# Performance work log

Measured on AMD Instinct MI355X. Metric: run time of the kernel, lower is better.

## Reference

```python
import jax, jax.numpy as jnp
import numpy as np
import math

B, S, D, H, DFF = 2, 2048, 1024, 16, 4096
DK = D // H
EPS = 1e-5


def setup_inputs() -> dict:
    key = jax.random.key(0)
    ks = jax.random.split(key, 8)
    s = 0.02
    return {
        "x": jax.random.normal(ks[0], (B, S, D), jnp.float32),
        "wq": jax.random.normal(ks[1], (D, D), jnp.float32) * s,
        "bq": jnp.zeros((D,), jnp.float32),
        "wk": jax.random.normal(ks[2], (D, D), jnp.float32) * s,
        "bk": jnp.zeros((D,), jnp.float32),
        "wv": jax.random.normal(ks[3], (D, D), jnp.float32) * s,
        "bv": jnp.zeros((D,), jnp.float32),
        "wo": jax.random.normal(ks[4], (D, D), jnp.float32) * s,
        "bo": jnp.zeros((D,), jnp.float32),
        "g1": jnp.ones((D,), jnp.float32),
        "beta1": jnp.zeros((D,), jnp.float32),
        "w1": jax.random.normal(ks[5], (D, DFF), jnp.float32) * s,
        "b1": jnp.zeros((DFF,), jnp.float32),
        "w2": jax.random.normal(ks[6], (DFF, D), jnp.float32) * s,
        "b2": jnp.zeros((D,), jnp.float32),
        "g2": jnp.ones((D,), jnp.float32),
        "beta2": jnp.zeros((D,), jnp.float32),
    }


def _layernorm(x, g, b):
    m = jnp.mean(x, axis=-1, keepdims=True)
    v = jnp.mean(jnp.square(x - m), axis=-1, keepdims=True)
    return (x - m) * jax.lax.rsqrt(v + EPS) * g + b


def reference(x, wq, bq, wk, bk, wv, bv, wo, bo, g1, beta1, w1, b1, w2, b2, g2, beta2):
    b, s, _ = x.shape
    # QKV projections -> [b, h, s, dk]
    q = (x @ wq + bq).reshape(b, s, H, DK).transpose(0, 2, 1, 3)
    k = (x @ wk + bk).reshape(b, s, H, DK).transpose(0, 2, 1, 3)
    v = (x @ wv + bv).reshape(b, s, H, DK).transpose(0, 2, 1, 3)
    scores = jnp.einsum('bhqd,bhkd->bhqk', q, k) / math.sqrt(DK)  # [b,h,s,s]
    # Faithful to source: softmax over dim=1 (heads axis), not the key axis.
    attn = jax.nn.softmax(scores, axis=1)
    ctx = jnp.einsum('bhqk,bhkd->bhqd', attn, v)
    ctx = ctx.transpose(0, 2, 1, 3).reshape(b, s, D)
    attn_out = ctx @ wo + bo
    # dropout is identity in eval mode
    x1 = _layernorm(x + attn_out, g1, beta1)
    ff = jax.nn.relu(x1 @ w1 + b1) @ w2 + b2
    return _layernorm(x1 + ff, g2, beta2)
```

## Files before the change

### kernel.cpp

```cpp
#include <hip/hip_runtime.h>
#include <stdint.h>

#define B_   2
#define S_   2048
#define D_   1024
#define H_   16
#define DK_  64
#define DFF_ 4096
#define M_   (B_ * S_)
#define QKV_LD 3072

typedef unsigned short u16;
typedef unsigned int   u32;
typedef __attribute__((ext_vector_type(8))) short short8;
typedef __attribute__((ext_vector_type(4))) float f32x4;

__device__ __forceinline__ float b2f(u16 u) {
  union { u32 i; float f; } z; z.i = ((u32)u) << 16; return z.f;
}
__device__ __forceinline__ u16 f2b(float f) {
  union { float f; u32 i; } z; z.f = f;
  u32 x = z.i;
  u32 r = (x + 0x7fffu + ((x >> 16) & 1u)) >> 16;
  return (u16)r;
}
__device__ __forceinline__ void load4(const float* p, float* f) {
  float4 v = *(const float4*)p;
  f[0] = v.x; f[1] = v.y; f[2] = v.z; f[3] = v.w;
}
__device__ __forceinline__ void load4(const u16* p, float* f) {
  uint2 v = *(const uint2*)p;
  f[0] = b2f(v.x & 0xffffu); f[1] = b2f(v.x >> 16);
  f[2] = b2f(v.y & 0xffffu); f[3] = b2f(v.y >> 16);
}
__device__ __forceinline__ void tstore(float* p, float v) { *p = v; }
__device__ __forceinline__ void tstore(u16* p, float v)   { *p = f2b(v); }

__device__ __forceinline__ void gld_lds16(const void* g, void* l) {
  __builtin_amdgcn_global_load_lds(
      (const __attribute__((address_space(1))) void*)g,
      (__attribute__((address_space(3))) void*)l, 16, 0, 0);
}

template<int BM, bool RELU, bool RES, bool BIAS, bool QKV, typename TO>
__global__ __launch_bounds__(256)
void gemm_bf16(const u16* __restrict__ A, const u16* __restrict__ Wt,
               const float* __restrict__ bias0, const float* __restrict__ bias1,
               const float* __restrict__ bias2, const float* __restrict__ res,
               TO* __restrict__ C, int M, int N, int K)
{
  constexpr int WM = BM / 2;
  constexpr int MI = WM / 16;
  __shared__ u16 As[BM][32];
  __shared__ u16 Bs[128][32];

  const int tid  = threadIdx.x;
  const int wave = tid >> 6;
  const int lane = tid & 63;
  const int lo16 = lane & 15;
  const int quad = lane >> 4;
  const int row0 = blockIdx.y * BM;
  const int col0 = blockIdx.x * 128;
  const int mb   = (wave & 1) * WM;
  const int nb   = (wave >> 1) * 64;

  const float* bias = bias0;
  float osc = 1.0f;
  if (QKV) {
    const int seg = col0 >> 10;
    bias = (seg == 0) ? bias0 : (seg == 1 ? bias1 : bias2);
    if (seg == 0) osc = 0.125f;
  }
  const int bc0 = QKV ? (col0 & 1023) : col0;

  f32x4 acc[MI][4];
#pragma unroll
  for (int i = 0; i < MI; ++i)
#pragma unroll
    for (int j = 0; j < 4; ++j) acc[i][j] = (f32x4){0.f, 0.f, 0.f, 0.f};

  const int s_row = tid >> 2;
  const int s_ch  = (tid & 3) * 8;
  const u16* gA = A  + (size_t)(row0 + s_row) * K + s_ch;
  const u16* gB = Wt + (size_t)(col0 + s_row) * K + s_ch;

  for (int k0 = 0; k0 < K; k0 += 32) {
    gld_lds16(gA, &As[s_row][s_ch]);
    if constexpr (BM == 128)
      gld_lds16(gA + (size_t)64 * K, &As[s_row + (BM == 128 ? 64 : 0)][s_ch]);
    gld_lds16(gB, &Bs[s_row][s_ch]);
    gld_lds16(gB + (size_t)64 * K, &Bs[s_row + 64][s_ch]);
    gA += 32; gB += 32;
    __syncthreads();

    short8 af[MI], bf[4];
#pragma unroll
    for (int mi = 0; mi < MI; ++mi)
      af[mi] = *(const short8*)&As[mb + mi * 16 + lo16][quad * 8];
#pragma unroll
    for (int ni = 0; ni < 4; ++ni)
      bf[ni] = *(const short8*)&Bs[nb + ni * 16 + lo16][quad * 8];
#pragma unroll
    for (int mi = 0; mi < MI; ++mi)
#pragma unroll
      for (int ni = 0; ni < 4; ++ni)
        acc[mi][ni] = __builtin_amdgcn_mfma_f32_16x16x32_bf16(af[mi], bf[ni], acc[mi][ni], 0, 0, 0);
    __syncthreads();
  }

  float bv[4];
#pragma unroll
  for (int ni = 0; ni < 4; ++ni)
    bv[ni] = BIAS ? bias[bc0 + nb + ni * 16 + lo16] : 0.f;
#pragma unroll
  for (int mi = 0; mi < MI; ++mi) {
#pragma unroll
    for (int ni = 0; ni < 4; ++ni) {
      const int col = col0 + nb + ni * 16 + lo16;
#pragma unroll
      for (int r = 0; r < 4; ++r) {
        const int row = row0 + mb + mi * 16 + quad * 4 + r;
        float vv = (acc[mi][ni][r] + bv[ni]) * osc;
        if (RELU) vv = fmaxf(vv, 0.f);
        if (RES)  vv += res[(size_t)row * N + col];
        tstore(C + (size_t)row * N + col, vv);
      }
    }
  }
}

__global__ __launch_bounds__(256)
void cvt_f2b(const float* __restrict__ in, u16* __restrict__ out)
{
  const size_t i = ((size_t)blockIdx.x * 256 + threadIdx.x) * 8;
  float4 a = *(const float4*)(in + i);
  float4 b = *(const float4*)(in + i + 4);
  uint4 o;
  o.x = (u32)f2b(a.x) | ((u32)f2b(a.y) << 16);
  o.y = (u32)f2b(a.z) | ((u32)f2b(a.w) << 16);
  o.z = (u32)f2b(b.x) | ((u32)f2b(b.y) << 16);
  o.w = (u32)f2b(b.z) | ((u32)f2b(b.w) << 16);
  *(uint4*)(out + i) = o;
}

__global__ __launch_bounds__(256)
void merge_b16(const u16* __restrict__ p0, const u16* __restrict__ p1,
               u16* __restrict__ out)
{
  const size_t i = ((size_t)blockIdx.x * 256 + threadIdx.x) * 8;
  uint4 a = *(const uint4*)(p0 + i);
  uint4 b = *(const uint4*)(p1 + i);
  uint4 o;
  const u32* ap = (const u32*)&a;
  const u32* bp = (const u32*)&b;
  u32* op = (u32*)&o;
#pragma unroll
  for (int j = 0; j < 4; ++j) {
    float lo = b2f((u16)(ap[j] & 0xffffu)) + b2f((u16)(bp[j] & 0xffffu));
    float hi = b2f((u16)(ap[j] >> 16))     + b2f((u16)(bp[j] >> 16));
    op[j] = (u32)f2b(lo) | ((u32)f2b(hi) << 16);
  }
  *(uint4*)(out + i) = o;
}

__global__ __launch_bounds__(256)
void transpose_f2b(const float* __restrict__ in, u16* __restrict__ out,
                   int ld_in, int ld_out)
{
  __shared__ u16 tile[64][68];
  const int t  = threadIdx.x;
  const int r0 = blockIdx.x * 64;
  const int c0 = blockIdx.y * 64;
  const int rr = t >> 4;
  const int cc = (t & 15) * 4;
#pragma unroll
  for (int rep = 0; rep < 4; ++rep) {
    float4 v = *(const float4*)(in + (size_t)(r0 + rr + rep * 16) * ld_in + c0 + cc);
    tile[rr + rep * 16][cc + 0] = f2b(v.x);
    tile[rr + rep * 16][cc + 1] = f2b(v.y);
    tile[rr + rep * 16][cc + 2] = f2b(v.z);
    tile[rr + rep * 16][cc + 3] = f2b(v.w);
  }
  __syncthreads();
#pragma unroll
  for (int rep = 0; rep < 4; ++rep) {
    const int dr = rr + rep * 16;
    uint2 o;
    o.x = (u32)tile[cc + 0][dr] | ((u32)tile[cc + 1][dr] << 16);
    o.y = (u32)tile[cc + 2][dr] | ((u32)tile[cc + 3][dr] << 16);
    *(uint2*)(out + (size_t)(c0 + dr) * ld_out + r0 + cc) = o;
  }
}

__global__ __launch_bounds__(256)
void transpose_bf16(const u16* __restrict__ in, u16* __restrict__ out,
                    int ld_in, int ld_out)
{
  __shared__ u16 tile[64][68];
  const int t  = threadIdx.x;
  const int r0 = blockIdx.x * 64;
  const int c0 = blockIdx.y * 64;
  const int rr = t >> 4;
  const int cc = (t & 15) * 4;
#pragma unroll
  for (int rep = 0; rep < 4; ++rep) {
    uint2 vv = *(const uint2*)(in + (size_t)(r0 + rr + rep * 16) * ld_in + c0 + cc);
    *(uint2*)&tile[rr + rep * 16][cc] = vv;
  }
  __syncthreads();
#pragma unroll
  for (int rep = 0; rep < 4; ++rep) {
    const int dr = rr + rep * 16;
    uint2 o;
    o.x = (u32)tile[cc + 0][dr] | ((u32)tile[cc + 1][dr] << 16);
    o.y = (u32)tile[cc + 2][dr] | ((u32)tile[cc + 3][dr] << 16);
    *(uint2*)(out + (size_t)(c0 + dr) * ld_out + r0 + cc) = o;
  }
}

__device__ __forceinline__ short8 scale8(short8 a, f32x4 r0, f32x4 r1) {
  const u32* ap = (const u32*)&a;
  short8 o;
  u32* op = (u32*)&o;
#pragma unroll
  for (int i = 0; i < 4; ++i) {
    union { u32 u; float f; } lo, hi;
    lo.u = ap[i] << 16;
    hi.u = ap[i] & 0xffff0000u;
    float rl = (i < 2) ? r0[2 * i]     : r1[2 * i - 4];
    float rh = (i < 2) ? r0[2 * i + 1] : r1[2 * i - 3];
    lo.f *= rl;
    hi.f *= rh;
    op[i] = ((lo.u + 0x8000u) >> 16) | ((hi.u + 0x8000u) & 0xffff0000u);
  }
  return o;
}

__global__ __launch_bounds__(512, 2)
void attention_mfma(const u16* __restrict__ q, const u16* __restrict__ k,
                    const u16* __restrict__ vt, u16* __restrict__ partial)
{
  __shared__ __align__(16) u16 Ws[16][32][64];
  __shared__ __align__(16) float Rs[32][64];

  const int tid  = threadIdx.x;
  const int wave = tid >> 6;
  const int lane = tid & 63;
  const int lo16 = lane & 15;
  const int quad = lane >> 4;

  const int p     = blockIdx.x;
  const int g     = (p & 7) >> 1;
  const int batch = g >> 1;
  const int half  = g & 1;
  const int qt    = ((p >> 3) << 1) | (p & 1);
  const int qrow0 = batch * S_ + qt * 32;
  const int tbase = half * 1024;

  const int qg = wave >> 2;
  const int tg = wave & 3;
  const int h0 = wave * 2;

  const u16* qrow = q + (size_t)(qrow0 + qg * 16 + lo16) * QKV_LD + quad * 8;
  short8 qf[32];
#pragma unroll
  for (int h = 0; h < 16; ++h) {
    qf[2 * h]     = *(const short8*)(qrow + h * 64);
    qf[2 * h + 1] = *(const short8*)(qrow + h * 64 + 32);
  }

  f32x4 acc[2][2][4];
#pragma unroll
  for (int a = 0; a < 2; ++a)
#pragma unroll
    for (int b = 0; b < 2; ++b)
#pragma unroll
      for (int c = 0; c < 4; ++c) acc[a][b][c] = (f32x4){0.f, 0.f, 0.f, 0.f};

  const u16* kbase = k + (size_t)(batch * S_ + tbase + tg * 16 + lo16) * QKV_LD + quad * 8;
  const u16* vbase0 = vt + (size_t)batch * S_ + tbase + quad * 8;

  int pos_r[4], qabs_r[4];
#pragma unroll
  for (int r = 0; r < 4; ++r) {
    qabs_r[r] = qg * 16 + quad * 4 + r;
    pos_r[r]  = (tg * 16 + lo16) ^ ((qabs_r[r] & 7) << 3);
  }

  for (int s = 0; s < 16; ++s) {
    {
      const u16* krow = kbase + (size_t)(s * 64) * QKV_LD;
      float ssum[4] = {0.f, 0.f, 0.f, 0.f};
#pragma unroll
      for (int h = 0; h < 16; ++h) {
        short8 b0 = *(const short8*)(krow + h * 64);
        short8 b1 = *(const short8*)(krow + h * 64 + 32);
        f32x4 sg = (f32x4){0.f, 0.f, 0.f, 0.f};
        sg = __builtin_amdgcn_mfma_f32_16x16x32_bf16(qf[2 * h],     b0, sg, 0, 0, 0);
        sg = __builtin_amdgcn_mfma_f32_16x16x32_bf16(qf[2 * h + 1], b1, sg, 0, 0, 0);
#pragma unroll
        for (int r = 0; r < 4; ++r) {
          union { float f; u32 u; } e;
          e.f = __expf(sg[r]);
          ssum[r] += e.f;
          Ws[h][qabs_r[r]][pos_r[r]] = (u16)((e.u + 0x8000u) >> 16);
        }
      }
#pragma unroll
      for (int r = 0; r < 4; ++r)
        Rs[qabs_r[r]][pos_r[r]] = 1.0f / ssum[r];
    }
    __syncthreads();

#pragma unroll
    for (int kc = 0; kc < 2; ++kc) {
      const int kbaseT = kc * 32 + quad * 8;
      const int ksw    = kbaseT ^ ((lo16 & 7) << 3);
      f32x4 rv0a = *(const f32x4*)&Rs[lo16][ksw];
      f32x4 rv0b = *(const f32x4*)&Rs[lo16][ksw + 4];
      f32x4 rv1a = *(const f32x4*)&Rs[16 + lo16][ksw];
      f32x4 rv1b = *(const f32x4*)&Rs[16 + lo16][ksw + 4];
#pragma unroll
      for (int hh = 0; hh < 2; ++hh) {
        short8 sw0 = scale8(*(const short8*)&Ws[h0 + hh][lo16][ksw],      rv0a, rv0b);
        short8 sw1 = scale8(*(const short8*)&Ws[h0 + hh][16 + lo16][ksw], rv1a, rv1b);
#pragma unroll
        for (int dt = 0; dt < 4; ++dt) {
          short8 bv = *(const short8*)(vbase0 +
              (size_t)((h0 + hh) * 64 + dt * 16 + lo16) * M_ + s * 64 + kc * 32);
          acc[hh][0][dt] = __builtin_amdgcn_mfma_f32_16x16x32_bf16(sw0, bv, acc[hh][0][dt], 0, 0, 0);
          acc[hh][1][dt] = __builtin_amdgcn_mfma_f32_16x16x32_bf16(sw1, bv, acc[hh][1][dt], 0, 0, 0);
        }
      }
    }
    __syncthreads();
  }

  u16* pb = partial + (size_t)half * M_ * D_;
#pragma unroll
  for (int hh = 0; hh < 2; ++hh)
#pragma unroll
    for (int qgg = 0; qgg < 2; ++qgg)
#pragma unroll
      for (int dt = 0; dt < 4; ++dt)
#pragma unroll
        for (int r = 0; r < 4; ++r) {
          const int row = qrow0 + qgg * 16 + quad * 4 + r;
          const int col = (h0 + hh) * 64 + dt * 16 + lo16;
          pb[(size_t)row * D_ + col] = f2b(acc[hh][qgg][dt][r]);
        }
}

__device__ __forceinline__ float block_sum(float vv, float* sm) {
#pragma unroll
  for (int o = 32; o > 0; o >>= 1) vv += __shfl_down(vv, o);
  __syncthreads();
  if ((threadIdx.x & 63) == 0) sm[threadIdx.x >> 6] = vv;
  __syncthreads();
  return sm[0] + sm[1] + sm[2] + sm[3];
}

template<bool HAS_Y, bool AUX>
__global__ __launch_bounds__(256)
void add_ln(const float* __restrict__ x, const u16* __restrict__ y,
            const float* __restrict__ g, const float* __restrict__ bta,
            float* __restrict__ out, u16* __restrict__ aux)
{
  __shared__ float sm[4];
  const int row = blockIdx.x;
  const int t   = threadIdx.x;
  const size_t base = (size_t)row * D_ + t * 4;

  float s[4];
  load4(x + base, s);
  if (HAS_Y) {
    float yv[4];
    load4(y + base, yv);
    s[0] += yv[0]; s[1] += yv[1]; s[2] += yv[2]; s[3] += yv[3];
  }

  float loc = s[0] + s[1] + s[2] + s[3];
  float tot = block_sum(loc, sm);
  float mean = tot * (1.f / 1024.f);
  float d0 = s[0] - mean, d1 = s[1] - mean, d2 = s[2] - mean, d3 = s[3] - mean;
  float sq = d0 * d0 + d1 * d1 + d2 * d2 + d3 * d3;
  float tv = block_sum(sq, sm);
  float rstd = rsqrtf(tv * (1.f / 1024.f) + 1e-5f);

  float4 gv = *(const float4*)(g + t * 4);
  float4 bv = *(const float4*)(bta + t * 4);
  float o0 = d0 * rstd * gv.x + bv.x;
  float o1 = d1 * rstd * gv.y + bv.y;
  float o2 = d2 * rstd * gv.z + bv.z;
  float o3 = d3 * rstd * gv.w + bv.w;
  *(float4*)(out + base) = make_float4(o0, o1, o2, o3);
  if (AUX) {
    uint2 ov;
    ov.x = (u32)f2b(o0) | ((u32)f2b(o1) << 16);
    ov.y = (u32)f2b(o2) | ((u32)f2b(o3) << 16);
    *(uint2*)(aux + base) = ov;
  }
}

extern "C" void kernel_launch(void* const* d_in, const int* in_sizes, int n_in,
                              void* d_out, int out_size, void* d_ws, size_t ws_size,
                              hipStream_t stream) {
  const float* x     = (const float*)d_in[0];
  const float* wq    = (const float*)d_in[1];
  const float* bq    = (const float*)d_in[2];
  const float* wk    = (const float*)d_in[3];
  const float* bk    = (const float*)d_in[4];
  const float* wv    = (const float*)d_in[5];
  const float* bv    = (const float*)d_in[6];
  const float* wo    = (const float*)d_in[7];
  const float* bo    = (const float*)d_in[8];
  const float* g1    = (const float*)d_in[9];
  const float* beta1 = (const float*)d_in[10];
  const float* w1    = (const float*)d_in[11];
  const float* b1    = (const float*)d_in[12];
  const float* w2    = (const float*)d_in[13];
  const float* b2    = (const float*)d_in[14];
  const float* g2    = (const float*)d_in[15];
  const float* beta2 = (const float*)d_in[16];
  float* outF = (float*)d_out;

  char* wsb = (char*)d_ws;
  const size_t MiB = (size_t)1 << 20;
  u16* qkv   = (u16*)(wsb + 0);
  u16* wqkvt = (u16*)(wsb + 24 * MiB);
  u16* vt    = (u16*)(wsb + 24 * MiB);
  u16* ctx_b = (u16*)(wsb + 0);
  u16* ao    = (u16*)(wsb + 8 * MiB);
  u16* wot   = (u16*)(wsb + 16 * MiB);
  u16* x1b   = (u16*)(wsb + 0);
  u16* w1t   = (u16*)(wsb + 8 * MiB);
  u16* w2t   = (u16*)(wsb + 12 * MiB);
  u16* h1    = (u16*)(wsb + 16 * MiB);
  u16* xb    = (u16*)d_out;
  u16* part  = (u16*)d_out;
  float* x1  = outF;
  float* z   = outF;

  dim3 blk(256);
  cvt_f2b<<<dim3((M_ * D_) / (256 * 8)), blk, 0, stream>>>(x, xb);
  transpose_f2b<<<dim3(16, 16), blk, 0, stream>>>(wq, wqkvt,                 D_, D_);
  transpose_f2b<<<dim3(16, 16), blk, 0, stream>>>(wk, wqkvt + 1024 * 1024,   D_, D_);
  transpose_f2b<<<dim3(16, 16), blk, 0, stream>>>(wv, wqkvt + 2048 * 1024,   D_, D_);
  gemm_bf16<128, false, false, true, true, u16><<<dim3(QKV_LD / 128, M_ / 128), blk, 0, stream>>>(
      xb, wqkvt, bq, bk, bv, nullptr, qkv, M_, QKV_LD, D_);
  transpose_bf16<<<dim3(M_ / 64, 1024 / 64), blk, 0, stream>>>(qkv + 2048, vt, QKV_LD, M_);
  attention_mfma<<<dim3(256), dim3(512), 0, stream>>>(qkv, qkv + 1024, vt, part);
  merge_b16<<<dim3((M_ * D_) / (256 * 8)), blk, 0, stream>>>(part, part + (size_t)M_ * D_, ctx_b);
  transpose_f2b<<<dim3(16, 16), blk, 0, stream>>>(wo, wot, D_, D_);
  gemm_bf16<64, false, false, true, false, u16><<<dim3(D_ / 128, M_ / 64), blk, 0, stream>>>(
      ctx_b, wot, bo, nullptr, nullptr, nullptr, ao, M_, D_, D_);
  add_ln<true, true><<<dim3(M_), blk, 0, stream>>>(x, ao, g1, beta1, x1, x1b);
  transpose_f2b<<<dim3(16, 32), blk, 0, stream>>>(w1, w1t, DFF_, D_);
  transpose_f2b<<<dim3(32, 16), blk, 0, stream>>>(w2, w2t, D_, 2048);
  gemm_bf16<128, true, false, true, false, u16><<<dim3(2048 / 128, M_ / 128), blk, 0, stream>>>(
      x1b, w1t, b1, nullptr, nullptr, nullptr, h1, M_, 2048, D_);
  gemm_bf16<64, false, true, false, false, float><<<dim3(D_ / 128, M_ / 64), blk, 0, stream>>>(
      h1, w2t, nullptr, nullptr, nullptr, x1, z, M_, D_, 2048);
  transpose_f2b<<<dim3(16, 32), blk, 0, stream>>>(w1 + 2048, w1t, DFF_, D_);
  transpose_f2b<<<dim3(32, 16), blk, 0, stream>>>(w2 + (size_t)2048 * 1024, w2t, D_, 2048);
  gemm_bf16<128, true, false, true, false, u16><<<dim3(2048 / 128, M_ / 128), blk, 0, stream>>>(
      x1b, w1t, b1 + 2048, nullptr, nullptr, nullptr, h1, M_, 2048, D_);
  gemm_bf16<64, false, true, true, false, float><<<dim3(D_ / 128, M_ / 64), blk, 0, stream>>>(
      h1, w2t, b2, nullptr, nullptr, z, z, M_, D_, 2048);
  add_ln<false, false><<<dim3(M_), blk, 0, stream>>>(z, nullptr, g2, beta2, outF, nullptr);
}
```

Before: 594.4 us.

## Shrink attention blocks to 16 query rows and double-buffer softmax tiles

The attention kernel now launches 512 blocks of 256 threads instead of 256 blocks of 512. Each block handles 16 query rows, and each wave covers 4 heads instead of 2 heads by 2 row groups. The exp-weight and reciprocal shared-memory tiles are double-buffered, so the next key tile's QK MFMA and exp work is issued before the current tile's PV accumulation, with one barrier per iteration instead of two. This aims to overlap the two phases and use more CUs, at the cost of reading each K/V tile twice as often overall.

```diff
diff --git a/kernel.cpp b/kernel.cpp
--- a/kernel.cpp
+++ b/kernel.cpp
@@ -236,12 +236,12 @@
   return o;
 }
 
-__global__ __launch_bounds__(512, 2)
+__global__ __launch_bounds__(256, 2)
 void attention_mfma(const u16* __restrict__ q, const u16* __restrict__ k,
                     const u16* __restrict__ vt, u16* __restrict__ partial)
 {
-  __shared__ __align__(16) u16 Ws[16][32][64];
-  __shared__ __align__(16) float Rs[32][64];
+  __shared__ __align__(16) u16 Ws[2][16][16][64];
+  __shared__ __align__(16) float Rs[2][16][64];
 
   const int tid  = threadIdx.x;
   const int wave = tid >> 6;
@@ -254,14 +254,13 @@
   const int batch = g >> 1;
   const int half  = g & 1;
   const int qt    = ((p >> 3) << 1) | (p & 1);
-  const int qrow0 = batch * S_ + qt * 32;
+  const int qrow0 = batch * S_ + qt * 16;
   const int tbase = half * 1024;
 
-  const int qg = wave >> 2;
-  const int tg = wave & 3;
-  const int h0 = wave * 2;
-
-  const u16* qrow = q + (size_t)(qrow0 + qg * 16 + lo16) * QKV_LD + quad * 8;
+  const int tg = wave;
+  const int h0 = wave * 4;
+
+  const u16* qrow = q + (size_t)(qrow0 + lo16) * QKV_LD + quad * 8;
   short8 qf[32];
 #pragma unroll
   for (int h = 0; h < 16; ++h) {
@@ -269,67 +268,65 @@
     qf[2 * h + 1] = *(const short8*)(qrow + h * 64 + 32);
   }
 
-  f32x4 acc[2][2][4];
-#pragma unroll
-  for (int a = 0; a < 2; ++a)
-#pragma unroll
-    for (int b = 0; b < 2; ++b)
-#pragma unroll
-      for (int c = 0; c < 4; ++c) acc[a][b][c] = (f32x4){0.f, 0.f, 0.f, 0.f};
+  f32x4 acc[4][4];
+#pragma unroll
+  for (int a = 0; a < 4; ++a)
+#pragma unroll
+    for (int c = 0; c < 4; ++c) acc[a][c] = (f32x4){0.f, 0.f, 0.f, 0.f};
 
   const u16* kbase = k + (size_t)(batch * S_ + tbase + tg * 16 + lo16) * QKV_LD + quad * 8;
-  const u16* vbase0 = vt + (size_t)batch * S_ + tbase + quad * 8;
+  const u16* vb    = vt + (size_t)batch * S_ + tbase + quad * 8;
 
   int pos_r[4], qabs_r[4];
 #pragma unroll
   for (int r = 0; r < 4; ++r) {
-    qabs_r[r] = qg * 16 + quad * 4 + r;
+    qabs_r[r] = quad * 4 + r;
     pos_r[r]  = (tg * 16 + lo16) ^ ((qabs_r[r] & 7) << 3);
   }
 
+  auto phaseA = [&](int s, int buf) {
+    const u16* krow = kbase + (size_t)(s * 64) * QKV_LD;
+    float ssum[4] = {0.f, 0.f, 0.f, 0.f};
+#pragma unroll
+    for (int h = 0; h < 16; ++h) {
+      short8 b0 = *(const short8*)(krow + h * 64);
+      short8 b1 = *(const short8*)(krow + h * 64 + 32);
+      f32x4 sg = (f32x4){0.f, 0.f, 0.f, 0.f};
+      sg = __builtin_amdgcn_mfma_f32_16x16x32_bf16(qf[2 * h],     b0, sg, 0, 0, 0);
+      sg = __builtin_amdgcn_mfma_f32_16x16x32_bf16(qf[2 * h + 1], b1, sg, 0, 0, 0);
+#pragma unroll
+      for (int r = 0; r < 4; ++r) {
+        union { float f; u32 u; } e;
+        e.f = __expf(sg[r]);
+        ssum[r] += e.f;
+        Ws[buf][h][qabs_r[r]][pos_r[r]] = (u16)((e.u + 0x8000u) >> 16);
+      }
+    }
+#pragma unroll
+    for (int r = 0; r < 4; ++r)
+      Rs[buf][qabs_r[r]][pos_r[r]] = 1.0f / ssum[r];
+  };
+
+  phaseA(0, 0);
+  __syncthreads();
+
   for (int s = 0; s < 16; ++s) {
-    {
-      const u16* krow = kbase + (size_t)(s * 64) * QKV_LD;
-      float ssum[4] = {0.f, 0.f, 0.f, 0.f};
-#pragma unroll
-      for (int h = 0; h < 16; ++h) {
-        short8 b0 = *(const short8*)(krow + h * 64);
-        short8 b1 = *(const short8*)(krow + h * 64 + 32);
-        f32x4 sg = (f32x4){0.f, 0.f, 0.f, 0.f};
-        sg = __builtin_amdgcn_mfma_f32_16x16x32_bf16(qf[2 * h],     b0, sg, 0, 0, 0);
-        sg = __builtin_amdgcn_mfma_f32_16x16x32_bf16(qf[2 * h + 1], b1, sg, 0, 0, 0);
-#pragma unroll
-        for (int r = 0; r < 4; ++r) {
-          union { float f; u32 u; } e;
-          e.f = __expf(sg[r]);
-          ssum[r] += e.f;
-          Ws[h][qabs_r[r]][pos_r[r]] = (u16)((e.u + 0x8000u) >> 16);
-        }
-      }
-#pragma unroll
-      for (int r = 0; r < 4; ++r)
-        Rs[qabs_r[r]][pos_r[r]] = 1.0f / ssum[r];
-    }
-    __syncthreads();
+    const int buf = s & 1;
+    if (s < 15) phaseA(s + 1, buf ^ 1);
 
 #pragma unroll
     for (int kc = 0; kc < 2; ++kc) {
-      const int kbaseT = kc * 32 + quad * 8;
-      const int ksw    = kbaseT ^ ((lo16 & 7) << 3);
-      f32x4 rv0a = *(const f32x4*)&Rs[lo16][ksw];
-      f32x4 rv0b = *(const f32x4*)&Rs[lo16][ksw + 4];
-      f32x4 rv1a = *(const f32x4*)&Rs[16 + lo16][ksw];
-      f32x4 rv1b = *(const f32x4*)&Rs[16 + lo16][ksw + 4];
-#pragma unroll
-      for (int hh = 0; hh < 2; ++hh) {
-        short8 sw0 = scale8(*(const short8*)&Ws[h0 + hh][lo16][ksw],      rv0a, rv0b);
-        short8 sw1 = scale8(*(const short8*)&Ws[h0 + hh][16 + lo16][ksw], rv1a, rv1b);
+      const int ksw = (kc * 32 + quad * 8) ^ ((lo16 & 7) << 3);
+      f32x4 rva = *(const f32x4*)&Rs[buf][lo16][ksw];
+      f32x4 rvb = *(const f32x4*)&Rs[buf][lo16][ksw + 4];
+#pragma unroll
+      for (int hh = 0; hh < 4; ++hh) {
+        short8 aw = scale8(*(const short8*)&Ws[buf][h0 + hh][lo16][ksw], rva, rvb);
 #pragma unroll
         for (int dt = 0; dt < 4; ++dt) {
-          short8 bv = *(const short8*)(vbase0 +
+          short8 bv = *(const short8*)(vb +
               (size_t)((h0 + hh) * 64 + dt * 16 + lo16) * M_ + s * 64 + kc * 32);
-          acc[hh][0][dt] = __builtin_amdgcn_mfma_f32_16x16x32_bf16(sw0, bv, acc[hh][0][dt], 0, 0, 0);
-          acc[hh][1][dt] = __builtin_amdgcn_mfma_f32_16x16x32_bf16(sw1, bv, acc[hh][1][dt], 0, 0, 0);
+          acc[hh][dt] = __builtin_amdgcn_mfma_f32_16x16x32_bf16(aw, bv, acc[hh][dt], 0, 0, 0);
         }
       }
     }
@@ -338,17 +335,15 @@
 
   u16* pb = partial + (size_t)half * M_ * D_;
 #pragma unroll
-  for (int hh = 0; hh < 2; ++hh)
-#pragma unroll
-    for (int qgg = 0; qgg < 2; ++qgg)
-#pragma unroll
-      for (int dt = 0; dt < 4; ++dt)
-#pragma unroll
-        for (int r = 0; r < 4; ++r) {
-          const int row = qrow0 + qgg * 16 + quad * 4 + r;
-          const int col = (h0 + hh) * 64 + dt * 16 + lo16;
-          pb[(size_t)row * D_ + col] = f2b(acc[hh][qgg][dt][r]);
-        }
+  for (int hh = 0; hh < 4; ++hh)
+#pragma unroll
+    for (int dt = 0; dt < 4; ++dt)
+#pragma unroll
+      for (int r = 0; r < 4; ++r) {
+        const int row = qrow0 + quad * 4 + r;
+        const int col = (h0 + hh) * 64 + dt * 16 + lo16;
+        pb[(size_t)row * D_ + col] = f2b(acc[hh][dt][r]);
+      }
 }
 
 __device__ __forceinline__ float block_sum(float vv, float* sm) {
@@ -449,7 +444,7 @@
   gemm_bf16<128, false, false, true, true, u16><<<dim3(QKV_LD / 128, M_ / 128), blk, 0, stream>>>(
       xb, wqkvt, bq, bk, bv, nullptr, qkv, M_, QKV_LD, D_);
   transpose_bf16<<<dim3(M_ / 64, 1024 / 64), blk, 0, stream>>>(qkv + 2048, vt, QKV_LD, M_);
-  attention_mfma<<<dim3(256), dim3(512), 0, stream>>>(qkv, qkv + 1024, vt, part);
+  attention_mfma<<<dim3(512), dim3(256), 0, stream>>>(qkv, qkv + 1024, vt, part);
   merge_b16<<<dim3((M_ * D_) / (256 * 8)), blk, 0, stream>>>(part, part + (size_t)M_ * D_, ctx_b);
   transpose_f2b<<<dim3(16, 16), blk, 0, stream>>>(wo, wot, D_, D_);
   gemm_bf16<64, false, false, true, false, u16><<<dim3(D_ / 128, M_ / 64), blk, 0, stream>>>(
```

Result: slower. 657.5 us (+10.6%).

## Double-buffer attention score tiles and prefetch next K block during PV

Applied to the files above, without the earlier changes.

Splits the attention loop into a software pipeline. The exp-score tile and reciprocal sums for step s+1 are computed into a second LDS buffer while step s's buffer feeds the PV MFMAs, and next-step K fragments are loaded into registers before the PV work. This removes one barrier per iteration and aims to overlap K global loads and score MFMAs with PV compute. In exchange it doubles LDS use to about 147KB, which likely prevents two blocks per CU. It also adds 32 short8 registers of K fragments, which may cause spills.

```diff
diff --git a/kernel.cpp b/kernel.cpp
--- a/kernel.cpp
+++ b/kernel.cpp
@@ -240,8 +240,8 @@
 void attention_mfma(const u16* __restrict__ q, const u16* __restrict__ k,
                     const u16* __restrict__ vt, u16* __restrict__ partial)
 {
-  __shared__ __align__(16) u16 Ws[16][32][64];
-  __shared__ __align__(16) float Rs[32][64];
+  __shared__ __align__(16) u16 Ws[2][16][32][64];
+  __shared__ __align__(16) float Rs[2][32][64];
 
   const int tid  = threadIdx.x;
   const int wave = tid >> 6;
@@ -277,7 +277,7 @@
 #pragma unroll
       for (int c = 0; c < 4; ++c) acc[a][b][c] = (f32x4){0.f, 0.f, 0.f, 0.f};
 
-  const u16* kbase = k + (size_t)(batch * S_ + tbase + tg * 16 + lo16) * QKV_LD + quad * 8;
+  const u16* kbase  = k + (size_t)(batch * S_ + tbase + tg * 16 + lo16) * QKV_LD + quad * 8;
   const u16* vbase0 = vt + (size_t)batch * S_ + tbase + quad * 8;
 
   int pos_r[4], qabs_r[4];
@@ -287,43 +287,54 @@
     pos_r[r]  = (tg * 16 + lo16) ^ ((qabs_r[r] & 7) << 3);
   }
 
+  {
+    const u16* krow = kbase;
+    float ssum[4] = {0.f, 0.f, 0.f, 0.f};
+#pragma unroll
+    for (int h = 0; h < 16; ++h) {
+      short8 b0 = *(const short8*)(krow + h * 64);
+      short8 b1 = *(const short8*)(krow + h * 64 + 32);
+      f32x4 sg = (f32x4){0.f, 0.f, 0.f, 0.f};
+      sg = __builtin_amdgcn_mfma_f32_16x16x32_bf16(qf[2 * h],     b0, sg, 0, 0, 0);
+      sg = __builtin_amdgcn_mfma_f32_16x16x32_bf16(qf[2 * h + 1], b1, sg, 0, 0, 0);
+#pragma unroll
+      for (int r = 0; r < 4; ++r) {
+        union { float f; u32 u; } e;
+        e.f = __expf(sg[r]);
+        ssum[r] += e.f;
+        Ws[0][h][qabs_r[r]][pos_r[r]] = (u16)((e.u + 0x8000u) >> 16);
+      }
+    }
+#pragma unroll
+    for (int r = 0; r < 4; ++r)
+      Rs[0][qabs_r[r]][pos_r[r]] = 1.0f / ssum[r];
+  }
+  __syncthreads();
+
   for (int s = 0; s < 16; ++s) {
-    {
-      const u16* krow = kbase + (size_t)(s * 64) * QKV_LD;
-      float ssum[4] = {0.f, 0.f, 0.f, 0.f};
+    const int buf = s & 1;
+
+    short8 kf[32];
+    if (s < 15) {
+      const u16* krow = kbase + (size_t)((s + 1) * 64) * QKV_LD;
 #pragma unroll
       for (int h = 0; h < 16; ++h) {
-        short8 b0 = *(const short8*)(krow + h * 64);
-        short8 b1 = *(const short8*)(krow + h * 64 + 32);
-        f32x4 sg = (f32x4){0.f, 0.f, 0.f, 0.f};
-        sg = __builtin_amdgcn_mfma_f32_16x16x32_bf16(qf[2 * h],     b0, sg, 0, 0, 0);
-        sg = __builtin_amdgcn_mfma_f32_16x16x32_bf16(qf[2 * h + 1], b1, sg, 0, 0, 0);
-#pragma unroll
-        for (int r = 0; r < 4; ++r) {
-          union { float f; u32 u; } e;
-          e.f = __expf(sg[r]);
-          ssum[r] += e.f;
-          Ws[h][qabs_r[r]][pos_r[r]] = (u16)((e.u + 0x8000u) >> 16);
-        }
+        kf[2 * h]     = *(const short8*)(krow + h * 64);
+        kf[2 * h + 1] = *(const short8*)(krow + h * 64 + 32);
       }
-#pragma unroll
-      for (int r = 0; r < 4; ++r)
-        Rs[qabs_r[r]][pos_r[r]] = 1.0f / ssum[r];
     }
-    __syncthreads();
 
 #pragma unroll
     for (int kc = 0; kc < 2; ++kc) {
-      const int kbaseT = kc * 32 + quad * 8;
-      const int ksw    = kbaseT ^ ((lo16 & 7) << 3);
-      f32x4 rv0a = *(const f32x4*)&Rs[lo16][ksw];
-      f32x4 rv0b = *(const f32x4*)&Rs[lo16][ksw + 4];
-      f32x4 rv1a = *(const f32x4*)&Rs[16 + lo16][ksw];
-      f32x4 rv1b = *(const f32x4*)&Rs[16 + lo16][ksw + 4];
+      const int ksw = (kc * 32 + quad * 8) ^ ((lo16 & 7) << 3);
+      f32x4 rv0a = *(const f32x4*)&Rs[buf][lo16][ksw];
+      f32x4 rv0b = *(const f32x4*)&Rs[buf][lo16][ksw + 4];
+      f32x4 rv1a = *(const f32x4*)&Rs[buf][16 + lo16][ksw];
+      f32x4 rv1b = *(const f32x4*)&Rs[buf][16 + lo16][ksw + 4];
 #pragma unroll
       for (int hh = 0; hh < 2; ++hh) {
-        short8 sw0 = scale8(*(const short8*)&Ws[h0 + hh][lo16][ksw],      rv0a, rv0b);
-        short8 sw1 = scale8(*(const short8*)&Ws[h0 + hh][16 + lo16][ksw], rv1a, rv1b);
+        short8 sw0 = scale8(*(const short8*)&Ws[buf][h0 + hh][lo16][ksw],      rv0a, rv0b);
+        short8 sw1 = scale8(*(const short8*)&Ws[buf][h0 + hh][16 + lo16][ksw], rv1a, rv1b);
 #pragma unroll
         for (int dt = 0; dt < 4; ++dt) {
           short8 bv = *(const short8*)(vbase0 +
@@ -333,6 +344,27 @@
         }
       }
     }
+
+    if (s < 15) {
+      float ssum[4] = {0.f, 0.f, 0.f, 0.f};
+#pragma unroll
+      for (int h = 0; h < 16; ++h) {
+        f32x4 sg = (f32x4){0.f, 0.f, 0.f, 0.f};
+        sg = __builtin_amdgcn_mfma_f32_16x16x32_bf16(qf[2 * h],     kf[2 * h],     sg, 0, 0, 0);
+        sg = __builtin_amdgcn_mfma_f32_16x16x32_bf16(qf[2 * h + 1], kf[2 * h + 1], sg, 0, 0, 0);
+#pragma unroll
+        for (int r = 0; r < 4; ++r) {
+          union { float f; u32 u; } e;
+          e.f = __expf(sg[r]);
+          ssum[r] += e.f;
+          Ws[buf ^ 1][h][qabs_r[r]][pos_r[r]] = (u16)((e.u + 0x8000u) >> 16);
+        }
+      }
+#pragma unroll
+      for (int r = 0; r < 4; ++r)
+        Rs[buf ^ 1][qabs_r[r]][pos_r[r]] = 1.0f / ssum[r];
+    }
+
     __syncthreads();
   }
 
```

New measurement: 730.3 us. 22.9% more time.
